# Kernel optimization log

Hardware: AMD Instinct MI355X
Metric: run time of the kernel (lower is better)

## Reference

```python
import jax, jax.numpy as jnp
import numpy as np

B, T, K = 512, 1024, 48

def setup_inputs() -> dict:
    key = jax.random.key(0)
    k_em, k_tag, k_len, k_tr, k_st, k_en = jax.random.split(key, 6)
    emissions = jax.random.normal(k_em, (B, T, K), dtype=jnp.float32)
    tags = jax.random.randint(k_tag, (B, T), 0, K)
    lengths = jax.random.randint(k_len, (B,), T // 2, T + 1)
    mask = jnp.arange(T)[None, :] < lengths[:, None]  # [B, T] bool, left-contiguous, mask[:,0]=True
    transitions = jax.random.uniform(k_tr, (K, K), minval=-0.1, maxval=0.1, dtype=jnp.float32)
    start_transitions = jax.random.uniform(k_st, (K,), minval=-0.1, maxval=0.1, dtype=jnp.float32)
    end_transitions = jax.random.uniform(k_en, (K,), minval=-0.1, maxval=0.1, dtype=jnp.float32)
    return {"emissions": emissions, "tags": tags, "mask": mask,
            "transitions": transitions, "start_transitions": start_transitions,
            "end_transitions": end_transitions}

def _crf_log_likelihood(emissions, transitions, start_transitions, end_transitions, tags, mask):
    b_idx = jnp.arange(emissions.shape[0])
    maskf = mask.astype(emissions.dtype)
    # ---- numerator: score of gold path ----
    emit_scores = jnp.take_along_axis(emissions, tags[:, :, None], axis=2)[:, :, 0]  # [B, T]
    trans_scores = transitions[tags[:, :-1], tags[:, 1:]]  # [B, T-1], trans[prev, cur]
    score = start_transitions[tags[:, 0]] + emit_scores[:, 0]
    score = score + jnp.sum((emit_scores[:, 1:] + trans_scores) * maskf[:, 1:], axis=1)
    last_idx = jnp.sum(mask, axis=1).astype(jnp.int32) - 1
    score = score + end_transitions[tags[b_idx, last_idx]]
    # ---- denominator: log partition via forward algorithm ----
    # NOTE: faithful to source, which indexes transitions[cur, prev] here (transposed vs numerator)
    alpha0 = start_transitions[None, :] + emissions[:, 0]  # [B, K]
    es = jnp.swapaxes(emissions[:, 1:], 0, 1)  # [T-1, B, K]
    ms = jnp.swapaxes(mask[:, 1:], 0, 1)       # [T-1, B]
    def step(alpha, xm):
        e_t, m_t = xm
        # next[b, x] = LSE_y(alpha[b, y] + trans[x, y]) + e_t[b, x]
        nxt = jax.nn.logsumexp(alpha[:, None, :] + transitions[None, :, :], axis=2) + e_t
        alpha = jnp.where(m_t[:, None], nxt, alpha)
        return alpha, None
    alpha, _ = jax.lax.scan(step, alpha0, (es, ms))
    log_den = jax.nn.logsumexp(alpha + end_transitions[None, :], axis=1)  # [B]
    return score - log_den

def reference(emissions, tags, mask, transitions, start_transitions, end_transitions):
    return _crf_log_likelihood(emissions, transitions, start_transitions, end_transitions, tags, mask)
```

## Files before the change

kernel.cpp:

```cpp
#include <hip/hip_runtime.h>
#include <math.h>

#define BB 512
#define TT 1024
#define KK 48
#define SEG 33
#define PF 4
#define CENTER 6

typedef _Float16 f16x8 __attribute__((ext_vector_type(8)));
typedef _Float16 f16x4 __attribute__((ext_vector_type(4)));
typedef float    f32x4 __attribute__((ext_vector_type(4)));

#if __has_builtin(__builtin_amdgcn_mfma_f32_16x16x16f16)
#define HAVE_X16 1
#else
#define HAVE_X16 0
#endif

static constexpr float L2E = 1.4426950408889634f;
static constexpr float LN2 = 0.6931471805599453f;

__device__ __forceinline__ float wave_reduce_sum_f(float v) {
    #pragma unroll
    for (int m = 32; m >= 1; m >>= 1) v += __shfl_xor(v, m, 64);
    return v;
}
__device__ __forceinline__ int wave_reduce_sum_i(int v) {
    #pragma unroll
    for (int m = 32; m >= 1; m >>= 1) v += __shfl_xor(v, m, 64);
    return v;
}

__device__ __forceinline__ int count_L(const void* mask, int b, int lane, unsigned w0) {
    int c = 0;
    if (w0 == 1u) {
        const int* mp = (const int*)mask + (size_t)b * TT;
        for (int t = lane; t < TT; t += 64) c += (mp[t] != 0);
    } else if (w0 == 0x3f800000u) {
        const float* mp = (const float*)mask + (size_t)b * TT;
        for (int t = lane; t < TT; t += 64) c += (mp[t] != 0.0f);
    } else {
        const unsigned char* mp = (const unsigned char*)mask + (size_t)b * TT;
        for (int t = lane; t < TT; t += 64) c += (mp[t] != 0);
    }
    return wave_reduce_sum_i(c);
}

__device__ __forceinline__ f32x4 mfma32(f16x8 a, f16x8 b, f32x4 c) {
    return __builtin_amdgcn_mfma_f32_16x16x32_f16(a, b, c, 0, 0, 0);
}

__device__ __forceinline__ float max12(const f32x4* v) {
    float mx = 0.0f;
    #pragma unroll
    for (int m = 0; m < 3; ++m) {
        #pragma unroll
        for (int e = 0; e < 4; ++e) mx = fmaxf(mx, v[m][e]);
    }
    return mx;
}

template <int BWD>
__device__ void scan_mfma(
    const float* __restrict__ em, const float* __restrict__ transitions,
    const float* __restrict__ start_t, const float* __restrict__ end_t,
    int Lb, int lane, int wofs, float (*sh_V)[KK], float* sh_D)
{
    const int c = lane & 15;
    const int g = lane >> 4;
    const int i = wofs + c + (BWD ? 1 : 0);
    const int N = Lb - 1;
    const int base = N / SEG, rem = N % SEG;
    const bool extra = (i < rem);
    const int len  = base + (extra ? 1 : 0);
    const int a    = 1 + i * base + (extra ? i : rem);
    const int t0   = a + len - 1;

    f16x8 A0[3];
    #pragma unroll
    for (int r = 0; r < 3; ++r) {
        f16x8 fr;
        #pragma unroll
        for (int e = 0; e < 8; ++e) {
            const int k = 16 * (e >> 2) + 4 * g + (e & 3);
            const int j = 16 * r + c;
            fr[e] = (_Float16)exp2f((BWD ? transitions[k * KK + j]
                                         : transitions[j * KK + k]) * L2E);
        }
        A0[r] = fr;
    }
#if HAVE_X16
    f16x4 A1[3];
    #pragma unroll
    for (int r = 0; r < 3; ++r) {
        f16x4 fr;
        #pragma unroll
        for (int e = 0; e < 4; ++e) {
            const int k = 32 + 4 * g + e;
            const int j = 16 * r + c;
            fr[e] = (_Float16)exp2f((BWD ? transitions[k * KK + j]
                                         : transitions[j * KK + k]) * L2E);
        }
        A1[r] = fr;
    }
#else
    f16x8 A1[3];
    #pragma unroll
    for (int r = 0; r < 3; ++r) {
        f16x8 fr;
        #pragma unroll
        for (int e = 0; e < 8; ++e) {
            const int k = 32 + 16 * (e >> 2) + 4 * g + (e & 3);
            const int j = 16 * r + c;
            float tv = 0.0f;
            if (k < KK)
                tv = exp2f((BWD ? transitions[k * KK + j]
                                : transitions[j * KK + k]) * L2E);
            fr[e] = (_Float16)tv;
        }
        A1[r] = fr;
    }
#endif

    f32x4 braw[3];
    #pragma unroll
    for (int m = 0; m < 3; ++m) {
        f32x4 bv;
        #pragma unroll
        for (int e = 0; e < 4; ++e) {
            const int k = 16 * m + 4 * g + e;
            float u0;
            if (BWD) u0 = (i == SEG - 1) ? exp2f(end_t[k] * L2E) : 1.0f;
            else     u0 = (i == 0) ? exp2f((start_t[k] + em[k]) * L2E) : 1.0f;
            bv[e] = u0;
        }
        braw[m] = bv;
    }
    if (BWD) {
        const float* p0 = em + (size_t)t0 * KK + 4 * g;
        #pragma unroll
        for (int m = 0; m < 3; ++m) {
            const f32x4 ev = *(const f32x4*)(p0 + 16 * m);
            #pragma unroll
            for (int e = 0; e < 4; ++e) braw[m][e] *= exp2f(ev[e] * L2E);
        }
    }

    f32x4 buf[PF][3];
    #pragma unroll
    for (int k = 0; k < PF; ++k) {
        int t = BWD ? (t0 - 1 - k) : (a + k);
        t = t < 0 ? 0 : (t > TT - 1 ? TT - 1 : t);
        const float* p = em + (size_t)t * KK + 4 * g;
        #pragma unroll
        for (int m = 0; m < 3; ++m) buf[k][m] = *(const f32x4*)(p + 16 * m);
    }

    int D = 0, Dprev = 0;
    float mx = max12(braw);
    mx = fmaxf(mx, __shfl_xor(mx, 16));
    mx = fmaxf(mx, __shfl_xor(mx, 32));
    int dadj = (int)((__float_as_uint(mx) >> 23) & 0xFF) - 127 + CENTER;

    f16x8 B0;
#if HAVE_X16
    f16x4 B1;
#else
    f16x8 B1;
#endif
    B0 = (f16x8){(_Float16)braw[0][0], (_Float16)braw[0][1],
                 (_Float16)braw[0][2], (_Float16)braw[0][3],
                 (_Float16)braw[1][0], (_Float16)braw[1][1],
                 (_Float16)braw[1][2], (_Float16)braw[1][3]};
#if HAVE_X16
    B1 = (f16x4){(_Float16)braw[2][0], (_Float16)braw[2][1],
                 (_Float16)braw[2][2], (_Float16)braw[2][3]};
#else
    B1 = (f16x8){(_Float16)braw[2][0], (_Float16)braw[2][1],
                 (_Float16)braw[2][2], (_Float16)braw[2][3],
                 (_Float16)0, (_Float16)0, (_Float16)0, (_Float16)0};
#endif

    f32x4 C[3];

    auto STEP = [&](const f32x4* E) {
        #pragma unroll
        for (int r = 0; r < 3; ++r) {
            f32x4 z = {0.0f, 0.0f, 0.0f, 0.0f};
            z = mfma32(A0[r], B0, z);
#if HAVE_X16
            z = __builtin_amdgcn_mfma_f32_16x16x16f16(A1[r], B1, z, 0, 0, 0);
#else
            z = mfma32(A1[r], B1, z);
#endif
            C[r] = z;
        }
        const float nd = -(float)dadj;
        #pragma unroll
        for (int m = 0; m < 3; ++m) {
            #pragma unroll
            for (int e = 0; e < 4; ++e)
                braw[m][e] = C[m][e] * exp2f(fmaf(E[m][e], L2E, nd));
        }
        Dprev = D;
        D += dadj;
        float mx2 = max12(braw);
        mx2 = fmaxf(mx2, __shfl_xor(mx2, 16));
        mx2 = fmaxf(mx2, __shfl_xor(mx2, 32));
        dadj = (int)((__float_as_uint(mx2) >> 23) & 0xFF) - 127 + CENTER;
        B0 = (f16x8){(_Float16)braw[0][0], (_Float16)braw[0][1],
                     (_Float16)braw[0][2], (_Float16)braw[0][3],
                     (_Float16)braw[1][0], (_Float16)braw[1][1],
                     (_Float16)braw[1][2], (_Float16)braw[1][3]};
#if HAVE_X16
        B1 = (f16x4){(_Float16)braw[2][0], (_Float16)braw[2][1],
                     (_Float16)braw[2][2], (_Float16)braw[2][3]};
#else
        B1 = (f16x8){(_Float16)braw[2][0], (_Float16)braw[2][1],
                     (_Float16)braw[2][2], (_Float16)braw[2][3],
                     (_Float16)0, (_Float16)0, (_Float16)0, (_Float16)0};
#endif
    };

    int sb = 1;
    int tn = BWD ? (t0 - 1 - PF) : (a + PF);
    #pragma unroll 1
    for (; sb + PF - 1 <= base; sb += PF) {
        #pragma unroll
        for (int k = 0; k < PF; ++k) {
            STEP(buf[k]);
            int t = tn + (BWD ? -k : k);
            t = t < 0 ? 0 : (t > TT - 1 ? TT - 1 : t);
            const float* p = em + (size_t)t * KK + 4 * g;
            #pragma unroll
            for (int m = 0; m < 3; ++m) buf[k][m] = *(const f32x4*)(p + 16 * m);
        }
        tn += BWD ? -PF : PF;
    }
    const int lsteps = base - sb + 1;
    #pragma unroll
    for (int k = 0; k < PF - 1; ++k)
        if (k < lsteps) STEP(buf[k]);

    const int slot = wofs + c;
    #pragma unroll
    for (int r = 0; r < 3; ++r) {
        #pragma unroll
        for (int e = 0; e < 4; ++e)
            sh_V[slot][16 * r + 4 * g + e] = BWD ? C[r][e] : braw[r][e];
    }
    if (g == 0) sh_D[slot] = (float)(BWD ? Dprev : D);

    f32x4 epE[3];
    #pragma unroll
    for (int k = 0; k < PF; ++k) {
        if (k == lsteps) {
            epE[0] = buf[k][0]; epE[1] = buf[k][1]; epE[2] = buf[k][2];
        }
    }
    #pragma unroll
    for (int r = 0; r < 3; ++r) {
        f32x4 z = {0.0f, 0.0f, 0.0f, 0.0f};
        z = mfma32(A0[r], B0, z);
#if HAVE_X16
        z = __builtin_amdgcn_mfma_f32_16x16x16f16(A1[r], B1, z, 0, 0, 0);
#else
        z = mfma32(A1[r], B1, z);
#endif
        C[r] = z;
    }
    float Dx;
    if (BWD) {
        Dx = (float)D;
    } else {
        const float nd = -(float)dadj;
        #pragma unroll
        for (int m = 0; m < 3; ++m) {
            #pragma unroll
            for (int e = 0; e < 4; ++e)
                C[m][e] = C[m][e] * exp2f(fmaf(epE[m][e], L2E, nd));
        }
        Dx = (float)(D + dadj);
    }
    if (extra) {
        #pragma unroll
        for (int r = 0; r < 3; ++r) {
            #pragma unroll
            for (int e = 0; e < 4; ++e)
                sh_V[slot][16 * r + 4 * g + e] = C[r][e];
        }
        if (g == 0) sh_D[slot] = Dx;
    }
}

__global__ __launch_bounds__(320, 1) void crf_all(
    const float* __restrict__ emissions,
    const int*   __restrict__ tags,
    const void*  __restrict__ mask,
    const float* __restrict__ transitions,
    const float* __restrict__ start_t,
    const float* __restrict__ end_t,
    float*       __restrict__ out)
{
    const int b    = blockIdx.x;
    const int wid  = threadIdx.x >> 6;
    const int lane = threadIdx.x & 63;
    __shared__ float sh_F[SEG - 1][KK];
    __shared__ float sh_G[SEG - 1][KK];
    __shared__ float sh_DF[SEG - 1];
    __shared__ float sh_DG[SEG - 1];
    __shared__ float sh_sc;

    const unsigned w0 = *((const unsigned*)mask);
    const int L = count_L(mask, b, lane, w0);
    const float* em = emissions + (size_t)b * TT * KK;

    if (wid < 2) {
        scan_mfma<0>(em, transitions, start_t, end_t, L, lane, wid * 16, sh_F, sh_DF);
    } else if (wid < 4) {
        scan_mfma<1>(em, transitions, start_t, end_t, L, lane, (wid - 2) * 16, sh_G, sh_DG);
    } else {
        const int* tg = tags + (size_t)b * TT;
        float sc = 0.0f;
        for (int t = lane; t < TT; t += 64) {
            if (t < L) {
                const int tagt = tg[t];
                float term = em[(size_t)t * KK + tagt];
                term += (t == 0) ? start_t[tagt] : transitions[tg[t - 1] * KK + tagt];
                sc += term;
            }
        }
        sc = wave_reduce_sum_f(sc);
        if (lane == 0) sh_sc = sc + end_t[tg[L - 1]];
    }
    __syncthreads();

    if (wid == 0) {
        const int k = lane >> 1;
        const int q = lane & 1;
        float dot = 0.0f, ns = 0.0f;
        #pragma unroll
        for (int e = 0; e < 24; ++e) {
            const int j = q * 24 + e;
            const float f = sh_F[k][j];
            dot += sh_G[k][j] * f;
            ns  += f;
        }
        dot += __shfl_xor(dot, 1, 64);
        ns  += __shfl_xor(ns, 1, 64);
        float v = 0.0f;
        if (q == 0) {
            v = log2f(dot) + sh_DG[k];
            if (k >= 1) v -= log2f(ns);
        }
        const float acc = wave_reduce_sum_f(v);
        if (lane == 0) out[b] = sh_sc - LN2 * (acc + sh_DF[0]);
    }
}

extern "C" void kernel_launch(void* const* d_in, const int* in_sizes, int n_in,
                              void* d_out, int out_size, void* d_ws, size_t ws_size,
                              hipStream_t stream) {
    const float* emissions   = (const float*)d_in[0];
    const int*   tags        = (const int*)  d_in[1];
    const void*  mask        = (const void*) d_in[2];
    const float* transitions = (const float*)d_in[3];
    const float* start_t     = (const float*)d_in[4];
    const float* end_t       = (const float*)d_in[5];
    float* out = (float*)d_out;
    (void)d_ws; (void)ws_size;

    crf_all<<<BB, 320, 0, stream>>>(emissions, tags, mask, transitions,
                                    start_t, end_t, out);
}
```

Before: 172.0 us.

## Split numerator into separate kernel and combine results via workspace

Result: slower. 191.8 us (+11.5%).

```diff
diff --git a/kernel.cpp b/kernel.cpp
--- a/kernel.cpp
+++ b/kernel.cpp
@@ -294,14 +294,11 @@
     }
 }
 
-__global__ __launch_bounds__(320, 1) void crf_all(
-    const float* __restrict__ emissions,
-    const int*   __restrict__ tags,
-    const void*  __restrict__ mask,
+__global__ __launch_bounds__(256, 1) void crf_scan(
+    const float* __restrict__ emissions, const void* __restrict__ mask,
     const float* __restrict__ transitions,
-    const float* __restrict__ start_t,
-    const float* __restrict__ end_t,
-    float*       __restrict__ out)
+    const float* __restrict__ start_t, const float* __restrict__ end_t,
+    float* __restrict__ ws_d)
 {
     const int b    = blockIdx.x;
     const int wid  = threadIdx.x >> 6;
@@ -310,7 +307,6 @@
     __shared__ float sh_G[SEG - 1][KK];
     __shared__ float sh_DF[SEG - 1];
     __shared__ float sh_DG[SEG - 1];
-    __shared__ float sh_sc;
 
     const unsigned w0 = *((const unsigned*)mask);
     const int L = count_L(mask, b, lane, w0);
@@ -318,21 +314,8 @@
 
     if (wid < 2) {
         scan_mfma<0>(em, transitions, start_t, end_t, L, lane, wid * 16, sh_F, sh_DF);
-    } else if (wid < 4) {
+    } else {
         scan_mfma<1>(em, transitions, start_t, end_t, L, lane, (wid - 2) * 16, sh_G, sh_DG);
-    } else {
-        const int* tg = tags + (size_t)b * TT;
-        float sc = 0.0f;
-        for (int t = lane; t < TT; t += 64) {
-            if (t < L) {
-                const int tagt = tg[t];
-                float term = em[(size_t)t * KK + tagt];
-                term += (t == 0) ? start_t[tagt] : transitions[tg[t - 1] * KK + tagt];
-                sc += term;
-            }
-        }
-        sc = wave_reduce_sum_f(sc);
-        if (lane == 0) sh_sc = sc + end_t[tg[L - 1]];
     }
     __syncthreads();
 
@@ -355,8 +338,43 @@
             if (k >= 1) v -= log2f(ns);
         }
         const float acc = wave_reduce_sum_f(v);
-        if (lane == 0) out[b] = sh_sc - LN2 * (acc + sh_DF[0]);
-    }
+        if (lane == 0) ws_d[b] = LN2 * (acc + sh_DF[0]);
+    }
+}
+
+__global__ __launch_bounds__(64, 1) void crf_num(
+    const float* __restrict__ emissions, const int* __restrict__ tags,
+    const void* __restrict__ mask, const float* __restrict__ transitions,
+    const float* __restrict__ start_t, const float* __restrict__ end_t,
+    float* __restrict__ ws_s)
+{
+    const int lane = threadIdx.x;
+    const int b    = blockIdx.x;
+    const unsigned w0 = *((const unsigned*)mask);
+    const int L = count_L(mask, b, lane, w0);
+
+    const float* em = emissions + (size_t)b * TT * KK;
+    const int*   tg = tags      + (size_t)b * TT;
+
+    float sc = 0.0f;
+    for (int t = lane; t < TT; t += 64) {
+        if (t < L) {
+            const int tagt = tg[t];
+            float term = em[(size_t)t * KK + tagt];
+            term += (t == 0) ? start_t[tagt] : transitions[tg[t - 1] * KK + tagt];
+            sc += term;
+        }
+    }
+    sc = wave_reduce_sum_f(sc);
+    if (lane == 0) ws_s[b] = sc + end_t[tg[L - 1]];
+}
+
+__global__ __launch_bounds__(256) void crf_combine(
+    const float* __restrict__ ws_s, const float* __restrict__ ws_d,
+    float* __restrict__ out)
+{
+    const int i = blockIdx.x * 256 + threadIdx.x;
+    if (i < BB) out[i] = ws_s[i] - ws_d[i];
 }
 
 extern "C" void kernel_launch(void* const* d_in, const int* in_sizes, int n_in,
@@ -368,9 +386,13 @@
     const float* transitions = (const float*)d_in[3];
     const float* start_t     = (const float*)d_in[4];
     const float* end_t       = (const float*)d_in[5];
-    float* out = (float*)d_out;
-    (void)d_ws; (void)ws_size;
-
-    crf_all<<<BB, 320, 0, stream>>>(emissions, tags, mask, transitions,
-                                    start_t, end_t, out);
-}
+    float* out  = (float*)d_out;
+    float* ws_s = (float*)d_ws;
+    float* ws_d = ws_s + BB;
+
+    crf_scan<<<BB, 256, 0, stream>>>(emissions, mask, transitions,
+                                     start_t, end_t, ws_d);
+    crf_num<<<BB, 64, 0, stream>>>(emissions, tags, mask, transitions,
+                                   start_t, end_t, ws_s);
+    crf_combine<<<2, 256, 0, stream>>>(ws_s, ws_d, out);
+}
```
